# Kernel optimization log

Hardware: AMD Instinct MI355X
Metric: run time of the kernel (lower is better)

The kernel has to match this reference:

```python
import jax, jax.numpy as jnp
import numpy as np

N_NODES = 100000
N_EDGES = 1600000
D = 8                      # node_channels_in = [D, D]
PROD = D * D               # 64
MSG_DIM = 128
IN_MSG = 2 * PROD + 2 * 2 + 2 * 1   # 134
MSG_OUT = 2 * D            # 16
IN_EIG = 2 * D + 2 * D     # node_channels_sum + 2*D = 32


def setup_inputs() -> dict:
    key = jax.random.key(0)
    ks = jax.random.split(key, 12)
    a = jax.random.normal(ks[0], (N_NODES, D, D), dtype=jnp.float32)
    h_i = 0.5 * (a + jnp.swapaxes(a, -1, -2))  # symmetric so eigh is valid
    edge_index = jax.random.randint(ks[1], (2, N_EDGES), 0, N_NODES)
    node_params = jax.random.normal(ks[2], (N_NODES, 2), dtype=jnp.float32)
    edge_params = jax.random.normal(ks[3], (N_EDGES, 1), dtype=jnp.float32)
    s = 0.05
    return {
        "h_i": h_i,
        "node_params": node_params,
        "edge_params": edge_params,
        "W1": jax.random.normal(ks[4], (IN_MSG, MSG_DIM), dtype=jnp.float32) * s,
        "b1": jnp.zeros((MSG_DIM,), dtype=jnp.float32),
        "W2": jax.random.normal(ks[5], (MSG_DIM, MSG_OUT), dtype=jnp.float32) * s,
        "b2": jnp.zeros((MSG_OUT,), dtype=jnp.float32),
        "W3": jax.random.normal(ks[6], (IN_EIG, MSG_DIM), dtype=jnp.float32) * s,
        "b3": jnp.zeros((MSG_DIM,), dtype=jnp.float32),
        "W4": jax.random.normal(ks[7], (MSG_DIM, D), dtype=jnp.float32) * s,
        "b4": jnp.zeros((D,), dtype=jnp.float32),
        "edge_index": edge_index,
    }


def reference(h_i, node_params, edge_params, W1, b1, W2, b2, W3, b3, W4, b4, edge_index):
    sender = edge_index[0]
    receiver = edge_index[1]
    E = sender.shape[0]
    N = node_params.shape[0]

    # gather + flatten node states per edge: [E, D*D]
    h_s = h_i[sender].reshape(E, -1)
    h_r = h_i[receiver].reshape(E, -1)
    # faithful to torch: edge_params[edge_index] -> [2, E, 1] then view(E, -1) -> [E, 2]
    ep = edge_params[edge_index].reshape(E, -1)

    cat = jnp.concatenate(
        [h_s, h_r, node_params[sender], node_params[receiver], ep], axis=1
    )  # [E, 134]

    # phi_message_Real: Linear -> SiLU -> Linear -> SiLU
    hidden = jax.nn.silu(cat @ W1 + b1)          # [E, 128]
    I_ij = jax.nn.silu(hidden @ W2 + b2)         # [E, 16]

    # scatter_add over receiver
    agg = jax.ops.segment_sum(I_ij, receiver, num_segments=N)  # [N, 16]

    # eigh-based update
    eigvals, eigvecs = jnp.linalg.eigh(h_i)          # [N, D], [N, D, D]
    mags = jnp.linalg.norm(eigvecs, axis=-1)         # [N, D] (row norms, as torch.norm(dim=-1))

    feats = jnp.concatenate([agg, eigvals, mags], axis=1)  # [N, 32]
    lam = jax.nn.softmax(jax.nn.silu(feats @ W3 + b3) @ W4 + b4, axis=-1)  # [N, D]

    # V diag(lam) V^T  per node
    h_updated = jnp.einsum("nij,nj,nkj->nik", eigvecs, lam, eigvecs)
    return h_updated
```

## Files before the change

kernel.cpp:

```cpp
#include <hip/hip_runtime.h>
#include <math.h>

typedef __attribute__((ext_vector_type(8))) short bf16x8;
typedef __attribute__((ext_vector_type(4))) float f32x4;
typedef _Float16 half2v __attribute__((ext_vector_type(2)));
typedef _Float16 f16x8 __attribute__((ext_vector_type(8)));

__device__ __forceinline__ float silu(float x) {
    return x / (1.0f + __expf(-x));
}

__device__ __forceinline__ unsigned short f2bf(float x) {
    union { float f; unsigned u; } v; v.f = x;
    unsigned r = v.u + 0x7fffu + ((v.u >> 16) & 1u);
    return (unsigned short)(r >> 16);
}

__device__ __forceinline__ unsigned pack2(float a, float b) {
    return (unsigned)f2bf(a) | ((unsigned)f2bf(b) << 16);
}

__device__ __forceinline__ unsigned pack2h(float a, float b) {
    half2v h; h[0] = (_Float16)a; h[1] = (_Float16)b;
    return __builtin_bit_cast(unsigned, h);
}

__device__ __forceinline__ unsigned cvt_pk(float lo, float hi) {
    unsigned r;
    asm("v_cvt_pk_bf16_f32 %0, %1, %2" : "=v"(r) : "v"(lo), "v"(hi));
    return r;
}

__global__ __launch_bounds__(256)
void k_pre2(const float* __restrict__ h_i,
            const float* __restrict__ np,
            const float* __restrict__ ep,
            const int* __restrict__ eidx,
            const float* __restrict__ W1, const float* __restrict__ b1,
            unsigned short* __restrict__ SAB,
            unsigned* __restrict__ epk,
            float* __restrict__ agg,
            int N, int E)
{
    if (blockIdx.x >= 1024) {
        const int tid = (blockIdx.x - 1024) * 256 + threadIdx.x;
        const int gs = 512 * 256;
        float4 z4 = make_float4(0.f, 0.f, 0.f, 0.f);
        for (int i = tid; i < N * 4; i += gs)
            ((float4*)agg)[i] = z4;
        for (int i = tid; i < E; i += gs)
            epk[i] = pack2h(ep[eidx[2 * i]], ep[eidx[2 * i + 1]]);
        return;
    }

    const int t = threadIdx.x;
    const int lane = t & 63;
    const int wv = t >> 6;
    const int lr = lane & 15;
    const int lq = lane >> 4;

    bf16x8 aw[4][3];
    #pragma unroll
    for (int mf = 0; mf < 4; ++mf) {
        const int c = wv * 64 + mf * 16 + lr;
        const bool isA = c < 128;
        const int col = c & 127;
        #pragma unroll
        for (int ks = 0; ks < 3; ++ks) {
            bf16x8 w;
            #pragma unroll
            for (int j = 0; j < 8; ++j) {
                const int kl = lq * 8 + j;
                float v = 0.0f;
                if (ks < 2) {
                    const int kk = ks * 32 + kl;
                    v = W1[(size_t)(isA ? kk : 64 + kk) * 128 + col];
                } else if (kl < 2) {
                    v = W1[(size_t)((isA ? 128 : 130) + kl) * 128 + col];
                }
                w[j] = (short)f2bf(v);
            }
            aw[mf][ks] = w;
        }
    }
    float4 b1v[4];
    #pragma unroll
    for (int mf = 0; mf < 4; ++mf) {
        if (wv < 2) b1v[mf] = *(const float4*)&b1[wv * 64 + mf * 16 + lq * 4];
        else        b1v[mf] = make_float4(0.f, 0.f, 0.f, 0.f);
    }

    const int nTiles = (N + 15) / 16;
    for (int tile = blockIdx.x; tile < nTiles; tile += 1024) {
        const int n  = tile * 16 + lr;
        const int nc = (n < N) ? n : (N - 1);

        const float* hr = h_i + (size_t)nc * 64;
        bf16x8 B0, B1, B2;
        {
            float4 a0 = *(const float4*)&hr[lq * 8];
            float4 a1 = *(const float4*)&hr[lq * 8 + 4];
            float4 a2 = *(const float4*)&hr[32 + lq * 8];
            float4 a3 = *(const float4*)&hr[32 + lq * 8 + 4];
            unsigned u[4];
            u[0] = pack2(a0.x, a0.y); u[1] = pack2(a0.z, a0.w);
            u[2] = pack2(a1.x, a1.y); u[3] = pack2(a1.z, a1.w);
            B0 = __builtin_bit_cast(bf16x8, *(uint4*)u);
            u[0] = pack2(a2.x, a2.y); u[1] = pack2(a2.z, a2.w);
            u[2] = pack2(a3.x, a3.y); u[3] = pack2(a3.z, a3.w);
            B1 = __builtin_bit_cast(bf16x8, *(uint4*)u);
            unsigned z[4] = {0u, 0u, 0u, 0u};
            if (lq == 0) z[0] = pack2(np[2 * nc], np[2 * nc + 1]);
            B2 = __builtin_bit_cast(bf16x8, *(uint4*)z);
        }

        f32x4 acc[4];
        #pragma unroll
        for (int mf = 0; mf < 4; ++mf) {
            acc[mf] = (f32x4){0.f, 0.f, 0.f, 0.f};
            acc[mf] = __builtin_amdgcn_mfma_f32_16x16x32_bf16(aw[mf][0], B0, acc[mf], 0, 0, 0);
            acc[mf] = __builtin_amdgcn_mfma_f32_16x16x32_bf16(aw[mf][1], B1, acc[mf], 0, 0, 0);
            acc[mf] = __builtin_amdgcn_mfma_f32_16x16x32_bf16(aw[mf][2], B2, acc[mf], 0, 0, 0);
        }

        if (n < N) {
            unsigned short* row = SAB + (size_t)n * 256;
            #pragma unroll
            for (int mf = 0; mf < 4; ++mf) {
                uint2 u;
                u.x = pack2h(acc[mf][0] + b1v[mf].x, acc[mf][1] + b1v[mf].y);
                u.y = pack2h(acc[mf][2] + b1v[mf].z, acc[mf][3] + b1v[mf].w);
                *(uint2*)&row[wv * 64 + mf * 16 + lq * 4] = u;
            }
        }
    }
}

__global__ __launch_bounds__(256, 3)
void k_edge_v5(const unsigned short* __restrict__ SAB,
               const unsigned* __restrict__ epk,
               const int* __restrict__ eidx,
               const float* __restrict__ W1,
               const float* __restrict__ W2, const float* __restrict__ b2,
               float* __restrict__ agg,
               int N, int E)
{
    const int t = threadIdx.x;
    const int lane = t & 63;
    const int wv = t >> 6;
    const int lr = lane & 15;
    const int lq = lane >> 4;

    half2v wA[4][4], wB[4][4];
    #pragma unroll
    for (int ks = 0; ks < 4; ++ks)
        #pragma unroll
        for (int c = 0; c < 4; ++c) {
            const int d = ks * 32 + lq * 8 + 2 * c;
            half2v a; a[0] = (_Float16)W1[132 * 128 + d]; a[1] = (_Float16)W1[132 * 128 + d + 1];
            half2v b; b[0] = (_Float16)W1[133 * 128 + d]; b[1] = (_Float16)W1[133 * 128 + d + 1];
            wA[ks][c] = a; wB[ks][c] = b;
        }

    bf16x8 bw2[4];
    #pragma unroll
    for (int ks = 0; ks < 4; ++ks) {
        bf16x8 w;
        #pragma unroll
        for (int j = 0; j < 8; ++j) {
            const int k = ks * 32 + lq * 8 + j;
            w[j] = (short)f2bf(W2[(size_t)k * 16 + lr]);
        }
        bw2[ks] = w;
    }
    const float bias2 = b2[lr];

    const uint4* S4 = (const uint4*)SAB;
    const int nG = (E + 15) / 16;
    const int gstride = gridDim.x * 4;
    int g = blockIdx.x * 4 + wv;
    if (g >= nG) return;

    int s0, r0; unsigned ep0; int rc0[4];
    uint4 A0[4], B0[4];
    {
        const int eb = g * 16;
        const int e = eb + lr; const int ec = (e < E) ? e : (E - 1);
        s0 = eidx[ec]; r0 = eidx[E + ec]; ep0 = epk[ec];
        if (eb + 16 <= E) {
            const int4 rv = *(const int4*)&eidx[E + eb + lq * 4];
            rc0[0] = rv.x; rc0[1] = rv.y; rc0[2] = rv.z; rc0[3] = rv.w;
        } else {
            #pragma unroll
            for (int r2 = 0; r2 < 4; ++r2) {
                int e4 = eb + lq * 4 + r2;
                rc0[r2] = eidx[E + ((e4 < E) ? e4 : (E - 1))];
            }
        }
        const uint4* pa = S4 + (size_t)s0 * 32;
        const uint4* pb = S4 + (size_t)r0 * 32 + 16;
        #pragma unroll
        for (int ks = 0; ks < 4; ++ks) { A0[ks] = pa[ks * 4 + lq]; B0[ks] = pb[ks * 4 + lq]; }
    }

    for (; g < nG; g += gstride) {
        const int gn = g + gstride;
        const bool hn = gn < nG;

        int s1 = 0, r1 = 0; unsigned ep1 = 0; int rc1[4] = {0, 0, 0, 0};
        if (hn) {
            const int eb = gn * 16;
            const int e = eb + lr; const int ec = (e < E) ? e : (E - 1);
            s1 = eidx[ec]; r1 = eidx[E + ec]; ep1 = epk[ec];
            if (eb + 16 <= E) {
                const int4 rv = *(const int4*)&eidx[E + eb + lq * 4];
                rc1[0] = rv.x; rc1[1] = rv.y; rc1[2] = rv.z; rc1[3] = rv.w;
            } else {
                #pragma unroll
                for (int r2 = 0; r2 < 4; ++r2) {
                    int e4 = eb + lq * 4 + r2;
                    rc1[r2] = eidx[E + ((e4 < E) ? e4 : (E - 1))];
                }
            }
        }

        const unsigned elo = (ep0 & 0xffffu) | (ep0 << 16);
        const unsigned ehi = (ep0 >> 16) | (ep0 & 0xffff0000u);
        const half2v e0 = __builtin_bit_cast(half2v, elo);
        const half2v e1 = __builtin_bit_cast(half2v, ehi);

        bf16x8 af[4];
        #pragma unroll
        for (int ks = 0; ks < 4; ++ks) {
            unsigned w[4];
            const unsigned* ua = (const unsigned*)&A0[ks];
            const unsigned* ub = (const unsigned*)&B0[ks];
            #pragma unroll
            for (int c = 0; c < 4; ++c) {
                half2v v = __builtin_bit_cast(half2v, ua[c])
                         + __builtin_bit_cast(half2v, ub[c]);
                v = wA[ks][c] * e0 + v;
                v = wB[ks][c] * e1 + v;
                const float x0 = (float)v[0];
                const float x1 = (float)v[1];
                w[c] = cvt_pk(silu(x0), silu(x1));
            }
            af[ks] = __builtin_bit_cast(bf16x8, *(uint4*)w);
        }

        uint4 A1[4], B1[4];
        if (hn) {
            const uint4* pa = S4 + (size_t)s1 * 32;
            const uint4* pb = S4 + (size_t)r1 * 32 + 16;
            #pragma unroll
            for (int ks = 0; ks < 4; ++ks) { A1[ks] = pa[ks * 4 + lq]; B1[ks] = pb[ks * 4 + lq]; }
        }

        f32x4 acc = (f32x4){0.f, 0.f, 0.f, 0.f};
        #pragma unroll
        for (int ks = 0; ks < 4; ++ks)
            acc = __builtin_amdgcn_mfma_f32_16x16x32_bf16(af[ks], bw2[ks], acc, 0, 0, 0);

        const int eb = g * 16;
        if (eb + 16 <= E) {
            #pragma unroll
            for (int r2 = 0; r2 < 4; ++r2)
                atomicAdd(&agg[(size_t)rc0[r2] * 16 + lr], silu(acc[r2] + bias2));
        } else {
            #pragma unroll
            for (int r2 = 0; r2 < 4; ++r2)
                if (eb + lq * 4 + r2 < E)
                    atomicAdd(&agg[(size_t)rc0[r2] * 16 + lr], silu(acc[r2] + bias2));
        }

        if (hn) {
            s0 = s1; r0 = r1; ep0 = ep1;
            #pragma unroll
            for (int r2 = 0; r2 < 4; ++r2) rc0[r2] = rc1[r2];
            #pragma unroll
            for (int ks = 0; ks < 4; ++ks) { A0[ks] = A1[ks]; B0[ks] = B1[ks]; }
        }
    }
}

__host__ __device__ constexpr int tix(int i, int j) {
    return (i <= j) ? (i * 8 - (i * (i + 1)) / 2 + j)
                    : (j * 8 - (j * (j + 1)) / 2 + i);
}

template <int P, int Q>
__device__ __forceinline__ void jrot(float* T, float* V) {
    const float app = T[tix(P, P)];
    const float aqq = T[tix(Q, Q)];
    const float apq = T[tix(P, Q)];

    float theta = (aqq - app) / (2.0f * apq);
    float at = fabsf(theta);
    float tt = 1.0f / (at + sqrtf(at * at + 1.0f));
    tt = (theta < 0.0f) ? -tt : tt;
    float cc = __frsqrt_rn(tt * tt + 1.0f);
    float ss = tt * cc;

    const bool skip = !(fabsf(apq) > 1e-36f);
    const float c  = skip ? 1.0f : cc;
    const float s  = skip ? 0.0f : ss;
    const float tu = skip ? 0.0f : tt;

    #pragma unroll
    for (int k = 0; k < 8; ++k) {
        if (k == P || k == Q) continue;
        const float akp = T[tix(k, P)], akq = T[tix(k, Q)];
        T[tix(k, P)] = c * akp - s * akq;
        T[tix(k, Q)] = s * akp + c * akq;
    }
    T[tix(P, P)] = app - tu * apq;
    T[tix(Q, Q)] = aqq + tu * apq;
    T[tix(P, Q)] = 0.0f;

    #pragma unroll
    for (int k = 0; k < 8; ++k) {
        const float vp = V[k * 8 + P], vq = V[k * 8 + Q];
        V[k * 8 + P] = c * vp - s * vq;
        V[k * 8 + Q] = s * vp + c * vq;
    }
}

__device__ __forceinline__ void jacobi_sweep(float* T, float* V) {
    jrot<0,1>(T,V); jrot<0,2>(T,V); jrot<0,3>(T,V); jrot<0,4>(T,V);
    jrot<0,5>(T,V); jrot<0,6>(T,V); jrot<0,7>(T,V);
    jrot<1,2>(T,V); jrot<1,3>(T,V); jrot<1,4>(T,V); jrot<1,5>(T,V);
    jrot<1,6>(T,V); jrot<1,7>(T,V);
    jrot<2,3>(T,V); jrot<2,4>(T,V); jrot<2,5>(T,V); jrot<2,6>(T,V);
    jrot<2,7>(T,V);
    jrot<3,4>(T,V); jrot<3,5>(T,V); jrot<3,6>(T,V); jrot<3,7>(T,V);
    jrot<4,5>(T,V); jrot<4,6>(T,V); jrot<4,7>(T,V);
    jrot<5,6>(T,V); jrot<5,7>(T,V);
    jrot<6,7>(T,V);
}

#define CSWAP(a, b)                                                          \
    {                                                                        \
        bool sw = eig[a] > eig[b];                                           \
        float lo = sw ? eig[b] : eig[a];                                     \
        float hi = sw ? eig[a] : eig[b];                                     \
        eig[a] = lo; eig[b] = hi;                                            \
        _Pragma("unroll")                                                    \
        for (int k = 0; k < 8; ++k) {                                        \
            float va = V[k * 8 + a], vb = V[k * 8 + b];                      \
            V[k * 8 + a] = sw ? vb : va;                                     \
            V[k * 8 + b] = sw ? va : vb;                                     \
        }                                                                    \
    }

__global__ __launch_bounds__(128)
void k_node2h(const float* __restrict__ h_i,
              const float* __restrict__ agg,
              const float* __restrict__ W3, const float* __restrict__ b3,
              const float* __restrict__ W4, const float* __restrict__ b4,
              float* __restrict__ out, int N)
{
    __shared__ _Float16 fl[2][64][40];
    __shared__ _Float16 hl[2][16][136];
    __shared__ float    zl[2][64][8];

    const int t = threadIdx.x;
    const int lane = t & 63;
    const int wv = t >> 6;
    const int lr = lane & 15;
    const int lq = lane >> 4;

    const int n  = blockIdx.x * 128 + t;
    const int nc = (n < N) ? n : (N - 1);

    float T[36], V[64];
    {
        float A[64];
        const float4* src = (const float4*)(h_i + (size_t)nc * 64);
        #pragma unroll
        for (int i = 0; i < 16; ++i) ((float4*)A)[i] = src[i];
        #pragma unroll
        for (int i = 0; i < 8; ++i)
            #pragma unroll
            for (int j = 0; j < 8; ++j)
                if (i <= j) T[tix(i, j)] = A[i * 8 + j];
    }
    #pragma unroll
    for (int i = 0; i < 64; ++i) V[i] = 0.0f;
    #pragma unroll
    for (int i = 0; i < 8; ++i) V[i * 8 + i] = 1.0f;

    #pragma unroll 1
    for (int sw = 0; sw < 4; ++sw) jacobi_sweep(T, V);

    float eig[8];
    #pragma unroll
    for (int i = 0; i < 8; ++i) eig[i] = T[tix(i, i)];

    CSWAP(0,1) CSWAP(2,3) CSWAP(4,5) CSWAP(6,7)
    CSWAP(0,2) CSWAP(1,3) CSWAP(4,6) CSWAP(5,7)
    CSWAP(1,2) CSWAP(5,6)
    CSWAP(0,4) CSWAP(1,5) CSWAP(2,6) CSWAP(3,7)
    CSWAP(2,4) CSWAP(3,5)
    CSWAP(1,2) CSWAP(3,4) CSWAP(5,6)

    f16x8 w3f[8];
    #pragma unroll
    for (int nf = 0; nf < 8; ++nf) {
        f16x8 w;
        #pragma unroll
        for (int j = 0; j < 8; ++j)
            w[j] = (_Float16)W3[(size_t)(lq * 8 + j) * 128 + nf * 16 + lr];
        w3f[nf] = w;
    }
    f16x8 w4f[4];
    #pragma unroll
    for (int ks = 0; ks < 4; ++ks) {
        f16x8 w;
        #pragma unroll
        for (int j = 0; j < 8; ++j)
            w[j] = (lr < 8) ? (_Float16)W4[(size_t)(ks * 32 + lq * 8 + j) * 8 + lr]
                            : (_Float16)0.0f;
        w4f[ks] = w;
    }
    float b3v[8];
    #pragma unroll
    for (int nf = 0; nf < 8; ++nf) b3v[nf] = b3[nf * 16 + lr];
    const float b4v = (lr < 8) ? b4[lr] : 0.0f;

    {
        float f[32];
        const float4* ag = (const float4*)(agg + (size_t)nc * 16);
        #pragma unroll
        for (int i = 0; i < 4; ++i) {
            float4 v = ag[i];
            f[i * 4 + 0] = v.x; f[i * 4 + 1] = v.y;
            f[i * 4 + 2] = v.z; f[i * 4 + 3] = v.w;
        }
        #pragma unroll
        for (int i = 0; i < 8; ++i) f[16 + i] = eig[i];
        #pragma unroll
        for (int i = 0; i < 8; ++i) f[24 + i] = 1.0f;

        unsigned* dst = (unsigned*)&fl[wv][lane][0];
        #pragma unroll
        for (int i = 0; i < 16; ++i) dst[i] = pack2h(f[2 * i], f[2 * i + 1]);
    }
    __syncthreads();

    #pragma unroll 1
    for (int b = 0; b < 4; ++b) {
        const f16x8 a1 = *(const f16x8*)&fl[wv][b * 16 + lr][lq * 8];
        f32x4 acc1[8];
        #pragma unroll
        for (int nf = 0; nf < 8; ++nf) {
            acc1[nf] = (f32x4){0.f, 0.f, 0.f, 0.f};
            acc1[nf] = __builtin_amdgcn_mfma_f32_16x16x32_f16(a1, w3f[nf], acc1[nf], 0, 0, 0);
        }
        #pragma unroll
        for (int nf = 0; nf < 8; ++nf)
            #pragma unroll
            for (int r2 = 0; r2 < 4; ++r2) {
                const float x = acc1[nf][r2] + b3v[nf];
                hl[wv][lq * 4 + r2][nf * 16 + lr] = (_Float16)silu(x);
            }
        __syncthreads();

        f32x4 acc2 = (f32x4){0.f, 0.f, 0.f, 0.f};
        #pragma unroll
        for (int ks = 0; ks < 4; ++ks) {
            const f16x8 a2 = *(const f16x8*)&hl[wv][lr][ks * 32 + lq * 8];
            acc2 = __builtin_amdgcn_mfma_f32_16x16x32_f16(a2, w4f[ks], acc2, 0, 0, 0);
        }
        if (lr < 8) {
            #pragma unroll
            for (int r2 = 0; r2 < 4; ++r2)
                zl[wv][b * 16 + lq * 4 + r2][lr] = acc2[r2] + b4v;
        }
        __syncthreads();
    }

    float z[8];
    {
        float4 z0 = *(const float4*)&zl[wv][lane][0];
        float4 z1 = *(const float4*)&zl[wv][lane][4];
        z[0] = z0.x; z[1] = z0.y; z[2] = z0.z; z[3] = z0.w;
        z[4] = z1.x; z[5] = z1.y; z[6] = z1.z; z[7] = z1.w;
    }
    float m = z[0];
    #pragma unroll
    for (int o = 1; o < 8; ++o) m = fmaxf(m, z[o]);
    float lam[8], den = 0.0f;
    #pragma unroll
    for (int o = 0; o < 8; ++o) { lam[o] = __expf(z[o] - m); den += lam[o]; }
    const float inv = 1.0f / den;
    #pragma unroll
    for (int o = 0; o < 8; ++o) lam[o] *= inv;

    if (n < N) {
        float* orow = out + (size_t)n * 64;
        #pragma unroll
        for (int i = 0; i < 8; ++i) {
            float si[8];
            #pragma unroll
            for (int j = 0; j < 8; ++j) si[j] = lam[j] * V[i * 8 + j];
            float r[8];
            #pragma unroll
            for (int k = 0; k < 8; ++k) {
                float sum = 0.0f;
                #pragma unroll
                for (int j = 0; j < 8; ++j) sum += si[j] * V[k * 8 + j];
                r[k] = sum;
            }
            ((float4*)orow)[i * 2 + 0] = make_float4(r[0], r[1], r[2], r[3]);
            ((float4*)orow)[i * 2 + 1] = make_float4(r[4], r[5], r[6], r[7]);
        }
    }
}

#define CATS 168
#define HS   136
__global__ __launch_bounds__(256, 2)
void k_edge_v2(const float* __restrict__ h_i,
               const float* __restrict__ node_params,
               const float* __restrict__ edge_params,
               const float* __restrict__ W1, const float* __restrict__ b1,
               const float* __restrict__ W2, const float* __restrict__ b2,
               const int* __restrict__ eidx,
               float* __restrict__ agg,
               int N, int E)
{
    __shared__ unsigned short smem[23680];
    unsigned short* w1t = smem;
    unsigned short* w2t = smem + 128 * CATS;
    unsigned short* cat = smem;
    unsigned short* hid = smem + 64 * CATS;

    const int t = threadIdx.x;
    const int lane = t & 63;
    const int wv = t >> 6;
    const int wn = wv & 1;
    const int wm = wv >> 1;
    const int lr = lane & 15;
    const int lq = lane >> 4;

    for (int idx = t; idx < 128 * 80; idx += 256) {
        const int col = idx & 127, kp = idx >> 7;
        const int k0 = 2 * kp;
        float f0 = (k0     < 134) ? W1[(size_t)k0       * 128 + col] : 0.0f;
        float f1 = (k0 + 1 < 134) ? W1[(size_t)(k0 + 1) * 128 + col] : 0.0f;
        *(unsigned*)&w1t[col * CATS + k0] = pack2(f0, f1);
    }
    for (int idx = t; idx < 16 * 64; idx += 256) {
        const int col = idx & 15, kp = idx >> 4;
        const int k0 = 2 * kp;
        *(unsigned*)&w2t[col * HS + k0] =
            pack2(W2[(size_t)k0 * 16 + col], W2[(size_t)(k0 + 1) * 16 + col]);
    }
    __syncthreads();

    bf16x8 bw1[4][5];
    #pragma unroll
    for (int nf = 0; nf < 4; ++nf)
        #pragma unroll
        for (int ks = 0; ks < 5; ++ks)
            bw1[nf][ks] = *(const bf16x8*)&w1t[(wn * 64 + nf * 16 + lr) * CATS + ks * 32 + lq * 8];
    bf16x8 bw2[4];
    #pragma unroll
    for (int ks = 0; ks < 4; ++ks)
        bw2[ks] = *(const bf16x8*)&w2t[lr * HS + ks * 32 + lq * 8];

    float bias1[4];
    #pragma unroll
    for (int nf = 0; nf < 4; ++nf) bias1[nf] = b1[wn * 64 + nf * 16 + lr];
    const float bias2 = b2[lr];
    __syncthreads();

    const int el = t >> 2;
    const int p  = t & 3;

    const int nTiles = E / 64;
    for (int tile = blockIdx.x; tile < nTiles; tile += gridDim.x) {
        const int ebase = tile * 64;
        {
            const int eg  = ebase + el;
            const int egc = (eg < E) ? eg : (E - 1);
            const int s = eidx[egc];
            const int r = eidx[E + egc];
            const float4* hs = (const float4*)(h_i + (size_t)s * 64);
            const float4* hr = (const float4*)(h_i + (size_t)r * 64);
            unsigned short* crow = cat + el * CATS;
            #pragma unroll
            for (int m = 0; m < 8; ++m) {
                const int q = p + 4 * m;
                float4 v = (q < 16) ? hs[q] : hr[q - 16];
                uint2 u; u.x = pack2(v.x, v.y); u.y = pack2(v.z, v.w);
                *(uint2*)&crow[q * 4] = u;
            }
            if (p == 0) {
                const int i0 = eidx[2 * egc];
                const int i1 = eidx[2 * egc + 1];
                uint4 u;
                u.x = pack2(node_params[2 * s], node_params[2 * s + 1]);
                u.y = pack2(node_params[2 * r], node_params[2 * r + 1]);
                u.z = pack2(edge_params[i0], edge_params[i1]);
                u.w = 0u;
                *(uint4*)&crow[128] = u;
            } else {
                uint4 z; z.x = z.y = z.z = z.w = 0u;
                *(uint4*)&crow[136 + (p - 1) * 8] = z;
            }
        }
        __syncthreads();

        f32x4 acc[2][4];
        #pragma unroll
        for (int mf = 0; mf < 2; ++mf)
            #pragma unroll
            for (int nf = 0; nf < 4; ++nf)
                acc[mf][nf] = (f32x4){0.f, 0.f, 0.f, 0.f};

        const unsigned short* pa = cat + (wm * 32 + lr) * CATS + lq * 8;
        #pragma unroll
        for (int ks = 0; ks < 5; ++ks) {
            const bf16x8 a0 = *(const bf16x8*)(pa + ks * 32);
            const bf16x8 a1 = *(const bf16x8*)(pa + 16 * CATS + ks * 32);
            #pragma unroll
            for (int nf = 0; nf < 4; ++nf) {
                acc[0][nf] = __builtin_amdgcn_mfma_f32_16x16x32_bf16(a0, bw1[nf][ks], acc[0][nf], 0, 0, 0);
                acc[1][nf] = __builtin_amdgcn_mfma_f32_16x16x32_bf16(a1, bw1[nf][ks], acc[1][nf], 0, 0, 0);
            }
        }
        __syncthreads();

        #pragma unroll
        for (int mf = 0; mf < 2; ++mf)
            #pragma unroll
            for (int nf = 0; nf < 4; ++nf) {
                const float bb = bias1[nf];
                #pragma unroll
                for (int r2 = 0; r2 < 4; ++r2) {
                    const float x = acc[mf][nf][r2] + bb;
                    hid[(wm * 32 + mf * 16 + lq * 4 + r2) * HS + wn * 64 + nf * 16 + lr] =
                        f2bf(silu(x));
                }
            }
        __syncthreads();

        f32x4 acc2 = (f32x4){0.f, 0.f, 0.f, 0.f};
        const unsigned short* ph = hid + (wv * 16 + lr) * HS + lq * 8;
        #pragma unroll
        for (int ks = 0; ks < 4; ++ks)
            acc2 = __builtin_amdgcn_mfma_f32_16x16x32_bf16(
                *(const bf16x8*)(ph + ks * 32), bw2[ks], acc2, 0, 0, 0);

        #pragma unroll
        for (int r2 = 0; r2 < 4; ++r2) {
            const int eg2 = ebase + wv * 16 + lq * 4 + r2;
            if (eg2 < E) {
                const int rcv = eidx[E + eg2];
                const float v = silu(acc2[r2] + bias2);
                atomicAdd(&agg[(size_t)rcv * 16 + lr], v);
            }
        }
        __syncthreads();
    }
}

extern "C" void kernel_launch(void* const* d_in, const int* in_sizes, int n_in,
                              void* d_out, int out_size, void* d_ws, size_t ws_size,
                              hipStream_t stream) {
    const float* h_i  = (const float*)d_in[0];
    const float* npar = (const float*)d_in[1];
    const float* epar = (const float*)d_in[2];
    const float* W1   = (const float*)d_in[3];
    const float* b1   = (const float*)d_in[4];
    const float* W2   = (const float*)d_in[5];
    const float* b2   = (const float*)d_in[6];
    const float* W3   = (const float*)d_in[7];
    const float* b3   = (const float*)d_in[8];
    const float* W4   = (const float*)d_in[9];
    const float* b4   = (const float*)d_in[10];
    const int*   eidx = (const int*)d_in[11];

    const int N = in_sizes[0] / 64;
    const int E = in_sizes[11] / 2;

    const size_t aggB = (size_t)N * 16 * sizeof(float);
    size_t off = (aggB + 255) & ~(size_t)255;
    const size_t sabOff = off;                  off += (size_t)N * 256 * 2;
    off = (off + 255) & ~(size_t)255;
    const size_t epkOff = off;                  off += (size_t)E * 4;
    const size_t need = off;

    float* agg = (float*)d_ws;

    if (ws_size >= need) {
        unsigned short* SAB = (unsigned short*)((char*)d_ws + sabOff);
        unsigned* epk = (unsigned*)((char*)d_ws + epkOff);

        k_pre2<<<1536, 256, 0, stream>>>(h_i, npar, epar, eidx, W1, b1,
                                         SAB, epk, agg, N, E);
        k_edge_v5<<<2048, 256, 0, stream>>>(SAB, epk, eidx, W1, W2, b2,
                                            agg, N, E);
    } else {
        (void)hipMemsetAsync(agg, 0, aggB, stream);
        int blocks = E / 64;
        if (blocks > 768) blocks = 768;
        k_edge_v2<<<blocks, 256, 0, stream>>>(h_i, npar, epar, W1, b1, W2, b2,
                                              eidx, agg, N, E);
    }
    k_node2h<<<(N + 127) / 128, 128, 0, stream>>>(h_i, agg, W3, b3, W4, b4,
                                                  (float*)d_out, N);
}
```

Before: 264.1 us.

## Process two nodes per thread in node kernel with interleaved Jacobi sweeps

```diff
diff --git a/kernel.cpp b/kernel.cpp
--- a/kernel.cpp
+++ b/kernel.cpp
@@ -289,56 +289,71 @@
 }
 
 template <int P, int Q>
-__device__ __forceinline__ void jrot(float* T, float* V) {
-    const float app = T[tix(P, P)];
-    const float aqq = T[tix(Q, Q)];
-    const float apq = T[tix(P, Q)];
-
-    float theta = (aqq - app) / (2.0f * apq);
-    float at = fabsf(theta);
-    float tt = 1.0f / (at + sqrtf(at * at + 1.0f));
-    tt = (theta < 0.0f) ? -tt : tt;
-    float cc = __frsqrt_rn(tt * tt + 1.0f);
-    float ss = tt * cc;
-
-    const bool skip = !(fabsf(apq) > 1e-36f);
-    const float c  = skip ? 1.0f : cc;
-    const float s  = skip ? 0.0f : ss;
-    const float tu = skip ? 0.0f : tt;
+__device__ __forceinline__ void jrot2(float* TA, float* VA, float* TB, float* VB) {
+    const float appA = TA[tix(P, P)], aqqA = TA[tix(Q, Q)], apqA = TA[tix(P, Q)];
+    const float appB = TB[tix(P, P)], aqqB = TB[tix(Q, Q)], apqB = TB[tix(P, Q)];
+
+    float thA = (aqqA - appA) / (2.0f * apqA);
+    float thB = (aqqB - appB) / (2.0f * apqB);
+    float atA = fabsf(thA), atB = fabsf(thB);
+    float ttA = 1.0f / (atA + sqrtf(atA * atA + 1.0f));
+    float ttB = 1.0f / (atB + sqrtf(atB * atB + 1.0f));
+    ttA = (thA < 0.0f) ? -ttA : ttA;
+    ttB = (thB < 0.0f) ? -ttB : ttB;
+    float ccA = __frsqrt_rn(ttA * ttA + 1.0f);
+    float ccB = __frsqrt_rn(ttB * ttB + 1.0f);
+    float ssA = ttA * ccA, ssB = ttB * ccB;
+
+    const bool skA = !(fabsf(apqA) > 1e-36f);
+    const bool skB = !(fabsf(apqB) > 1e-36f);
+    const float cA = skA ? 1.0f : ccA, sA = skA ? 0.0f : ssA, tuA = skA ? 0.0f : ttA;
+    const float cB = skB ? 1.0f : ccB, sB = skB ? 0.0f : ssB, tuB = skB ? 0.0f : ttB;
 
     #pragma unroll
     for (int k = 0; k < 8; ++k) {
         if (k == P || k == Q) continue;
-        const float akp = T[tix(k, P)], akq = T[tix(k, Q)];
-        T[tix(k, P)] = c * akp - s * akq;
-        T[tix(k, Q)] = s * akp + c * akq;
-    }
-    T[tix(P, P)] = app - tu * apq;
-    T[tix(Q, Q)] = aqq + tu * apq;
-    T[tix(P, Q)] = 0.0f;
+        const float akpA = TA[tix(k, P)], akqA = TA[tix(k, Q)];
+        TA[tix(k, P)] = cA * akpA - sA * akqA;
+        TA[tix(k, Q)] = sA * akpA + cA * akqA;
+        const float akpB = TB[tix(k, P)], akqB = TB[tix(k, Q)];
+        TB[tix(k, P)] = cB * akpB - sB * akqB;
+        TB[tix(k, Q)] = sB * akpB + cB * akqB;
+    }
+    TA[tix(P, P)] = appA - tuA * apqA;
+    TA[tix(Q, Q)] = aqqA + tuA * apqA;
+    TA[tix(P, Q)] = 0.0f;
+    TB[tix(P, P)] = appB - tuB * apqB;
+    TB[tix(Q, Q)] = aqqB + tuB * apqB;
+    TB[tix(P, Q)] = 0.0f;
 
     #pragma unroll
     for (int k = 0; k < 8; ++k) {
-        const float vp = V[k * 8 + P], vq = V[k * 8 + Q];
-        V[k * 8 + P] = c * vp - s * vq;
-        V[k * 8 + Q] = s * vp + c * vq;
-    }
-}
-
-__device__ __forceinline__ void jacobi_sweep(float* T, float* V) {
-    jrot<0,1>(T,V); jrot<0,2>(T,V); jrot<0,3>(T,V); jrot<0,4>(T,V);
-    jrot<0,5>(T,V); jrot<0,6>(T,V); jrot<0,7>(T,V);
-    jrot<1,2>(T,V); jrot<1,3>(T,V); jrot<1,4>(T,V); jrot<1,5>(T,V);
-    jrot<1,6>(T,V); jrot<1,7>(T,V);
-    jrot<2,3>(T,V); jrot<2,4>(T,V); jrot<2,5>(T,V); jrot<2,6>(T,V);
-    jrot<2,7>(T,V);
-    jrot<3,4>(T,V); jrot<3,5>(T,V); jrot<3,6>(T,V); jrot<3,7>(T,V);
-    jrot<4,5>(T,V); jrot<4,6>(T,V); jrot<4,7>(T,V);
-    jrot<5,6>(T,V); jrot<5,7>(T,V);
-    jrot<6,7>(T,V);
-}
-
-#define CSWAP(a, b)                                                          \
+        const float vpA = VA[k * 8 + P], vqA = VA[k * 8 + Q];
+        VA[k * 8 + P] = cA * vpA - sA * vqA;
+        VA[k * 8 + Q] = sA * vpA + cA * vqA;
+        const float vpB = VB[k * 8 + P], vqB = VB[k * 8 + Q];
+        VB[k * 8 + P] = cB * vpB - sB * vqB;
+        VB[k * 8 + Q] = sB * vpB + cB * vqB;
+    }
+}
+
+__device__ __forceinline__ void jacobi_sweep2(float* TA, float* VA,
+                                              float* TB, float* VB) {
+    jrot2<0,1>(TA,VA,TB,VB); jrot2<0,2>(TA,VA,TB,VB); jrot2<0,3>(TA,VA,TB,VB);
+    jrot2<0,4>(TA,VA,TB,VB); jrot2<0,5>(TA,VA,TB,VB); jrot2<0,6>(TA,VA,TB,VB);
+    jrot2<0,7>(TA,VA,TB,VB);
+    jrot2<1,2>(TA,VA,TB,VB); jrot2<1,3>(TA,VA,TB,VB); jrot2<1,4>(TA,VA,TB,VB);
+    jrot2<1,5>(TA,VA,TB,VB); jrot2<1,6>(TA,VA,TB,VB); jrot2<1,7>(TA,VA,TB,VB);
+    jrot2<2,3>(TA,VA,TB,VB); jrot2<2,4>(TA,VA,TB,VB); jrot2<2,5>(TA,VA,TB,VB);
+    jrot2<2,6>(TA,VA,TB,VB); jrot2<2,7>(TA,VA,TB,VB);
+    jrot2<3,4>(TA,VA,TB,VB); jrot2<3,5>(TA,VA,TB,VB); jrot2<3,6>(TA,VA,TB,VB);
+    jrot2<3,7>(TA,VA,TB,VB);
+    jrot2<4,5>(TA,VA,TB,VB); jrot2<4,6>(TA,VA,TB,VB); jrot2<4,7>(TA,VA,TB,VB);
+    jrot2<5,6>(TA,VA,TB,VB); jrot2<5,7>(TA,VA,TB,VB);
+    jrot2<6,7>(TA,VA,TB,VB);
+}
+
+#define CSWAPG(eig, V, a, b)                                                 \
     {                                                                        \
         bool sw = eig[a] > eig[b];                                           \
         float lo = sw ? eig[b] : eig[a];                                     \
@@ -352,8 +367,16 @@
         }                                                                    \
     }
 
+#define SORT8(eig, V)                                                        \
+    CSWAPG(eig,V,0,1) CSWAPG(eig,V,2,3) CSWAPG(eig,V,4,5) CSWAPG(eig,V,6,7)  \
+    CSWAPG(eig,V,0,2) CSWAPG(eig,V,1,3) CSWAPG(eig,V,4,6) CSWAPG(eig,V,5,7)  \
+    CSWAPG(eig,V,1,2) CSWAPG(eig,V,5,6)                                      \
+    CSWAPG(eig,V,0,4) CSWAPG(eig,V,1,5) CSWAPG(eig,V,2,6) CSWAPG(eig,V,3,7)  \
+    CSWAPG(eig,V,2,4) CSWAPG(eig,V,3,5)                                      \
+    CSWAPG(eig,V,1,2) CSWAPG(eig,V,3,4) CSWAPG(eig,V,5,6)
+
 __global__ __launch_bounds__(128)
-void k_node2h(const float* __restrict__ h_i,
+void k_node2x(const float* __restrict__ h_i,
               const float* __restrict__ agg,
               const float* __restrict__ W3, const float* __restrict__ b3,
               const float* __restrict__ W4, const float* __restrict__ b4,
@@ -362,6 +385,8 @@
     __shared__ _Float16 fl[2][64][40];
     __shared__ _Float16 hl[2][16][136];
     __shared__ float    zl[2][64][8];
+    __shared__ float    vstash[128][65];
+    __shared__ float    estash[128][9];
 
     const int t = threadIdx.x;
     const int lane = t & 63;
@@ -369,39 +394,53 @@
     const int lr = lane & 15;
     const int lq = lane >> 4;
 
-    const int n  = blockIdx.x * 128 + t;
-    const int nc = (n < N) ? n : (N - 1);
-
-    float T[36], V[64];
+    const int nA  = blockIdx.x * 256 + t;
+    const int nB  = nA + 128;
+    const int ncA = (nA < N) ? nA : (N - 1);
+    const int ncB = (nB < N) ? nB : (N - 1);
+
+    float TA[36], VA[64], TB[36], VB[64];
     {
         float A[64];
-        const float4* src = (const float4*)(h_i + (size_t)nc * 64);
+        const float4* src = (const float4*)(h_i + (size_t)ncA * 64);
         #pragma unroll
         for (int i = 0; i < 16; ++i) ((float4*)A)[i] = src[i];
         #pragma unroll
         for (int i = 0; i < 8; ++i)
             #pragma unroll
             for (int j = 0; j < 8; ++j)
-                if (i <= j) T[tix(i, j)] = A[i * 8 + j];
-    }
-    #pragma unroll
-    for (int i = 0; i < 64; ++i) V[i] = 0.0f;
-    #pragma unroll
-    for (int i = 0; i < 8; ++i) V[i * 8 + i] = 1.0f;
+                if (i <= j) TA[tix(i, j)] = A[i * 8 + j];
+    }
+    {
+        float A[64];
+        const float4* src = (const float4*)(h_i + (size_t)ncB * 64);
+        #pragma unroll
+        for (int i = 0; i < 16; ++i) ((float4*)A)[i] = src[i];
+        #pragma unroll
+        for (int i = 0; i < 8; ++i)
+            #pragma unroll
+            for (int j = 0; j < 8; ++j)
+                if (i <= j) TB[tix(i, j)] = A[i * 8 + j];
+    }
+    #pragma unroll
+    for (int i = 0; i < 64; ++i) { VA[i] = 0.0f; VB[i] = 0.0f; }
+    #pragma unroll
+    for (int i = 0; i < 8; ++i) { VA[i * 8 + i] = 1.0f; VB[i * 8 + i] = 1.0f; }
 
     #pragma unroll 1
-    for (int sw = 0; sw < 4; ++sw) jacobi_sweep(T, V);
-
-    float eig[8];
-    #pragma unroll
-    for (int i = 0; i < 8; ++i) eig[i] = T[tix(i, i)];
-
-    CSWAP(0,1) CSWAP(2,3) CSWAP(4,5) CSWAP(6,7)
-    CSWAP(0,2) CSWAP(1,3) CSWAP(4,6) CSWAP(5,7)
-    CSWAP(1,2) CSWAP(5,6)
-    CSWAP(0,4) CSWAP(1,5) CSWAP(2,6) CSWAP(3,7)
-    CSWAP(2,4) CSWAP(3,5)
-    CSWAP(1,2) CSWAP(3,4) CSWAP(5,6)
+    for (int sw = 0; sw < 4; ++sw) jacobi_sweep2(TA, VA, TB, VB);
+
+    float eigA[8], eigB[8];
+    #pragma unroll
+    for (int i = 0; i < 8; ++i) { eigA[i] = TA[tix(i, i)]; eigB[i] = TB[tix(i, i)]; }
+
+    SORT8(eigA, VA)
+    SORT8(eigB, VB)
+
+    #pragma unroll
+    for (int i = 0; i < 64; ++i) vstash[t][i] = VB[i];
+    #pragma unroll
+    for (int i = 0; i < 8; ++i) estash[t][i] = eigB[i];
 
     f16x8 w3f[8];
     #pragma unroll
@@ -427,93 +466,108 @@
     for (int nf = 0; nf < 8; ++nf) b3v[nf] = b3[nf * 16 + lr];
     const float b4v = (lr < 8) ? b4[lr] : 0.0f;
 
-    {
-        float f[32];
-        const float4* ag = (const float4*)(agg + (size_t)nc * 16);
-        #pragma unroll
-        for (int i = 0; i < 4; ++i) {
-            float4 v = ag[i];
-            f[i * 4 + 0] = v.x; f[i * 4 + 1] = v.y;
-            f[i * 4 + 2] = v.z; f[i * 4 + 3] = v.w;
-        }
-        #pragma unroll
-        for (int i = 0; i < 8; ++i) f[16 + i] = eig[i];
-        #pragma unroll
-        for (int i = 0; i < 8; ++i) f[24 + i] = 1.0f;
-
-        unsigned* dst = (unsigned*)&fl[wv][lane][0];
-        #pragma unroll
-        for (int i = 0; i < 16; ++i) dst[i] = pack2h(f[2 * i], f[2 * i + 1]);
-    }
-    __syncthreads();
-
     #pragma unroll 1
-    for (int b = 0; b < 4; ++b) {
-        const f16x8 a1 = *(const f16x8*)&fl[wv][b * 16 + lr][lq * 8];
-        f32x4 acc1[8];
-        #pragma unroll
-        for (int nf = 0; nf < 8; ++nf) {
-            acc1[nf] = (f32x4){0.f, 0.f, 0.f, 0.f};
-            acc1[nf] = __builtin_amdgcn_mfma_f32_16x16x32_f16(a1, w3f[nf], acc1[nf], 0, 0, 0);
-        }
-        #pragma unroll
-        for (int nf = 0; nf < 8; ++nf)
-            #pragma unroll
-            for (int r2 = 0; r2 < 4; ++r2) {
-                const float x = acc1[nf][r2] + b3v[nf];
-                hl[wv][lq * 4 + r2][nf * 16 + lr] = (_Float16)silu(x);
-            }
+    for (int pass = 0; pass < 2; ++pass) {
+        const int n  = pass ? nB : nA;
+        const int nc = pass ? ncB : ncA;
+        float* V   = VA;
+        float* eig = eigA;
+        if (pass) {
+            #pragma unroll
+            for (int i = 0; i < 64; ++i) V[i] = vstash[t][i];
+            #pragma unroll
+            for (int i = 0; i < 8; ++i) eig[i] = estash[t][i];
+        }
+
+        {
+            float f[32];
+            const float4* ag = (const float4*)(agg + (size_t)nc * 16);
+            #pragma unroll
+            for (int i = 0; i < 4; ++i) {
+                float4 v = ag[i];
+                f[i * 4 + 0] = v.x; f[i * 4 + 1] = v.y;
+                f[i * 4 + 2] = v.z; f[i * 4 + 3] = v.w;
+            }
+            #pragma unroll
+            for (int i = 0; i < 8; ++i) f[16 + i] = eig[i];
+            #pragma unroll
+            for (int i = 0; i < 8; ++i) f[24 + i] = 1.0f;
+
+            unsigned* dst = (unsigned*)&fl[wv][lane][0];
+            #pragma unroll
+            for (int i = 0; i < 16; ++i) dst[i] = pack2h(f[2 * i], f[2 * i + 1]);
+        }
         __syncthreads();
 
-        f32x4 acc2 = (f32x4){0.f, 0.f, 0.f, 0.f};
-        #pragma unroll
-        for (int ks = 0; ks < 4; ++ks) {
-            const f16x8 a2 = *(const f16x8*)&hl[wv][lr][ks * 32 + lq * 8];
-            acc2 = __builtin_amdgcn_mfma_f32_16x16x32_f16(a2, w4f[ks], acc2, 0, 0, 0);
-        }
-        if (lr < 8) {
-            #pragma unroll
-            for (int r2 = 0; r2 < 4; ++r2)
-                zl[wv][b * 16 + lq * 4 + r2][lr] = acc2[r2] + b4v;
+        #pragma unroll 1
+        for (int b = 0; b < 4; ++b) {
+            const f16x8 a1 = *(const f16x8*)&fl[wv][b * 16 + lr][lq * 8];
+            f32x4 acc1[8];
+            #pragma unroll
+            for (int nf = 0; nf < 8; ++nf) {
+                acc1[nf] = (f32x4){0.f, 0.f, 0.f, 0.f};
+                acc1[nf] = __builtin_amdgcn_mfma_f32_16x16x32_f16(a1, w3f[nf], acc1[nf], 0, 0, 0);
+            }
+            #pragma unroll
+            for (int nf = 0; nf < 8; ++nf)
+                #pragma unroll
+                for (int r2 = 0; r2 < 4; ++r2) {
+                    const float x = acc1[nf][r2] + b3v[nf];
+                    hl[wv][lq * 4 + r2][nf * 16 + lr] = (_Float16)silu(x);
+                }
+            __syncthreads();
+
+            f32x4 acc2 = (f32x4){0.f, 0.f, 0.f, 0.f};
+            #pragma unroll
+            for (int ks = 0; ks < 4; ++ks) {
+                const f16x8 a2 = *(const f16x8*)&hl[wv][lr][ks * 32 + lq * 8];
+                acc2 = __builtin_amdgcn_mfma_f32_16x16x32_f16(a2, w4f[ks], acc2, 0, 0, 0);
+            }
+            if (lr < 8) {
+                #pragma unroll
+                for (int r2 = 0; r2 < 4; ++r2)
+                    zl[wv][b * 16 + lq * 4 + r2][lr] = acc2[r2] + b4v;
+            }
+            __syncthreads();
+        }
+
+        float z[8];
+        {
+            float4 z0 = *(const float4*)&zl[wv][lane][0];
+            float4 z1 = *(const float4*)&zl[wv][lane][4];
+            z[0] = z0.x; z[1] = z0.y; z[2] = z0.z; z[3] = z0.w;
+            z[4] = z1.x; z[5] = z1.y; z[6] = z1.z; z[7] = z1.w;
+        }
+        float m = z[0];
+        #pragma unroll
+        for (int o = 1; o < 8; ++o) m = fmaxf(m, z[o]);
+        float lam[8], den = 0.0f;
+        #pragma unroll
+        for (int o = 0; o < 8; ++o) { lam[o] = __expf(z[o] - m); den += lam[o]; }
+        const float inv = 1.0f / den;
+        #pragma unroll
+        for (int o = 0; o < 8; ++o) lam[o] *= inv;
+
+        if (n < N) {
+            float* orow = out + (size_t)n * 64;
+            #pragma unroll
+            for (int i = 0; i < 8; ++i) {
+                float si[8];
+                #pragma unroll
+                for (int j = 0; j < 8; ++j) si[j] = lam[j] * V[i * 8 + j];
+                float r[8];
+                #pragma unroll
+                for (int k = 0; k < 8; ++k) {
+                    float sum = 0.0f;
+                    #pragma unroll
+                    for (int j = 0; j < 8; ++j) sum += si[j] * V[k * 8 + j];
+                    r[k] = sum;
+                }
+                ((float4*)orow)[i * 2 + 0] = make_float4(r[0], r[1], r[2], r[3]);
+                ((float4*)orow)[i * 2 + 1] = make_float4(r[4], r[5], r[6], r[7]);
+            }
         }
         __syncthreads();
-    }
-
-    float z[8];
-    {
-        float4 z0 = *(const float4*)&zl[wv][lane][0];
-        float4 z1 = *(const float4*)&zl[wv][lane][4];
-        z[0] = z0.x; z[1] = z0.y; z[2] = z0.z; z[3] = z0.w;
-        z[4] = z1.x; z[5] = z1.y; z[6] = z1.z; z[7] = z1.w;
-    }
-    float m = z[0];
-    #pragma unroll
-    for (int o = 1; o < 8; ++o) m = fmaxf(m, z[o]);
-    float lam[8], den = 0.0f;
-    #pragma unroll
-    for (int o = 0; o < 8; ++o) { lam[o] = __expf(z[o] - m); den += lam[o]; }
-    const float inv = 1.0f / den;
-    #pragma unroll
-    for (int o = 0; o < 8; ++o) lam[o] *= inv;
-
-    if (n < N) {
-        float* orow = out + (size_t)n * 64;
-        #pragma unroll
-        for (int i = 0; i < 8; ++i) {
-            float si[8];
-            #pragma unroll
-            for (int j = 0; j < 8; ++j) si[j] = lam[j] * V[i * 8 + j];
-            float r[8];
-            #pragma unroll
-            for (int k = 0; k < 8; ++k) {
-                float sum = 0.0f;
-                #pragma unroll
-                for (int j = 0; j < 8; ++j) sum += si[j] * V[k * 8 + j];
-                r[k] = sum;
-            }
-            ((float4*)orow)[i * 2 + 0] = make_float4(r[0], r[1], r[2], r[3]);
-            ((float4*)orow)[i * 2 + 1] = make_float4(r[4], r[5], r[6], r[7]);
-        }
     }
 }
 
@@ -709,6 +763,6 @@
         k_edge_v2<<<blocks, 256, 0, stream>>>(h_i, npar, epar, W1, b1, W2, b2,
                                               eidx, agg, N, E);
     }
-    k_node2h<<<(N + 127) / 128, 128, 0, stream>>>(h_i, agg, W3, b3, W4, b4,
+    k_node2x<<<(N + 255) / 256, 128, 0, stream>>>(h_i, agg, W3, b3, W4, b4,
                                                   (float*)d_out, N);
 }
```

Result: slower. 279.9 us (+6.0%).
